# Kernel optimization log

Hardware: AMD Instinct MI355X
Metric: run time of the kernel (lower is better)

Reference implementation:

```python
import jax, jax.numpy as jnp
import numpy as np

B, S, F = 32, 8, 4
N0, N1, N2 = 2048, 4096, 2048
H, OUT = 1024, 256
IN = N0 + N1 + N2  # 8192
SC_LAYERS = 2


def setup_inputs() -> dict:
    key = jax.random.key(0)
    ks = jax.random.split(key, 16)
    rn = jax.random.normal
    inp = {
        'xs0': rn(ks[0], (B, S, N0), jnp.float32),
        'xs1': rn(ks[1], (B, S, N1), jnp.float32),
        'xs2': rn(ks[2], (B, S, N2), jnp.float32),
        # dense Laplacians, scaled so L@x keeps unit-ish variance
        'L0': rn(ks[3], (N0, N0), jnp.float32) / np.sqrt(N0).astype(np.float32),
        'L1': rn(ks[4], (N1, N1), jnp.float32) / np.sqrt(N1).astype(np.float32),
        'L2': rn(ks[5], (N2, N2), jnp.float32) / np.sqrt(N2).astype(np.float32),
        # per-layer, per-filter diagonal weights (std=0.01 as in torch init)
        'Wc0': 0.01 * rn(ks[6], (SC_LAYERS, F, N0), jnp.float32),
        'Wc1': 0.01 * rn(ks[7], (SC_LAYERS, F, N1), jnp.float32),
        'Wc2': 0.01 * rn(ks[8], (SC_LAYERS, F, N2), jnp.float32),
        # MLP params (xavier-ish)
        'W_in': rn(ks[9], (IN, H), jnp.float32) / np.sqrt(IN).astype(np.float32),
        'b_in': jnp.zeros((H,), jnp.float32),
        'W_h': rn(ks[10], (H, H), jnp.float32) / np.sqrt(H).astype(np.float32),
        'b_h': jnp.zeros((H,), jnp.float32),
        'W_out': rn(ks[11], (H, OUT), jnp.float32) / np.sqrt(H).astype(np.float32),
        'b_out': jnp.zeros((OUT,), jnp.float32),
    }
    return inp


def _conv_stack(x, L, Wc):
    # x: [B, S, n]; L: [n, n]; Wc: [layers, F, n]
    for l in range(Wc.shape[0]):
        # batched Laplacian matmul: (L @ x_bs) for every (b, s)
        Lx = jnp.einsum('bsn,mn->bsm', x, L)  # [B, S, n]
        # diagonal filter scaling + activation + sum over filters (fused)
        x = jax.nn.relu(Lx[:, :, None, :] * Wc[l][None, None, :, :]).sum(axis=2)
    return x


def reference(xs0, xs1, xs2, L0, L1, L2, Wc0, Wc1, Wc2,
              W_in, b_in, W_h, b_h, W_out, b_out):
    h = jnp.concatenate([
        _conv_stack(xs0, L0, Wc0),
        _conv_stack(xs1, L1, Wc1),
        _conv_stack(xs2, L2, Wc2),
    ], axis=-1)                      # [B, S, IN]
    h = h.sum(axis=1)                # sum over sequence -> [B, IN]
    h = jax.nn.relu(h @ W_in + b_in)
    h = jax.nn.relu(h @ W_h + b_h)   # single hidden layer (nn_layers=2)
    return h @ W_out + b_out         # [B, OUT]
```

## Files before the change

### kernel.cpp

```cpp
#include <hip/hip_runtime.h>
#include <hip/hip_bf16.h>


#define B_    32
#define S_    8
#define BS_   256
#define F_    4
#define IN_   8192
#define H_    1024
#define OUT_  256

#define L_TOT  25165824LL
#define LOFF1  4194304LL
#define LOFF2  20971520LL

#define PF_B1  2097152LL
#define PF_B2  10485760LL
#define PF_TOT 12582912LL

typedef __attribute__((ext_vector_type(8)))  short bf16x8;
typedef __attribute__((ext_vector_type(4)))  short short4v;
typedef __attribute__((ext_vector_type(8)))  short short8v;
typedef __attribute__((ext_vector_type(16))) float f32x16;
typedef __attribute__((ext_vector_type(4)))  float f32x4;

typedef const __attribute__((address_space(1))) void* gas_ptr;
typedef __attribute__((address_space(3))) void* las_ptr;

__device__ __forceinline__ void gload16(const void* g, void* s) {
    __builtin_amdgcn_global_load_lds((gas_ptr)g, (las_ptr)s, 16, 0, 0);
}

__device__ __forceinline__ unsigned short rne_bf16(float f) {
    unsigned int u = __builtin_bit_cast(unsigned int, f);
    u += 0x7FFFu + ((u >> 16) & 1u);
    return (unsigned short)(u >> 16);
}

__global__ void k_pre(const float* __restrict__ L0, const float* __restrict__ L1,
                      const float* __restrict__ L2, unsigned short* __restrict__ Lb,
                      const float* __restrict__ x0, const float* __restrict__ x1,
                      const float* __restrict__ x2,
                      unsigned short* __restrict__ Xhi, unsigned short* __restrict__ Xlo,
                      const float* __restrict__ Wc0, const float* __restrict__ Wc1,
                      const float* __restrict__ Wc2, float* __restrict__ PM)
{
    const int bx = blockIdx.x, tid = threadIdx.x;
    if (bx < 3072) {
        const long long b0 = (long long)bx * 8192;
        const float* src; long long off;
        if (b0 < LOFF1)      { src = L0; off = 0; }
        else if (b0 < LOFF2) { src = L1; off = LOFF1; }
        else                 { src = L2; off = LOFF2; }
        const float* pb = src + (b0 - off) + tid * 8;
        #pragma unroll
        for (int u = 0; u < 4; ++u) {
            const float* p = pb + u * 2048;
            f32x4 a = __builtin_nontemporal_load((const f32x4*)p);
            f32x4 b = __builtin_nontemporal_load((const f32x4*)p + 1);
            short8v o;
            o[0] = (short)rne_bf16(a.x); o[1] = (short)rne_bf16(a.y);
            o[2] = (short)rne_bf16(a.z); o[3] = (short)rne_bf16(a.w);
            o[4] = (short)rne_bf16(b.x); o[5] = (short)rne_bf16(b.y);
            o[6] = (short)rne_bf16(b.z); o[7] = (short)rne_bf16(b.w);
            *(short8v*)(Lb + b0 + u * 2048 + tid * 8) = o;
        }
    } else if (bx < 3584) {
        const int base = (bx - 3072) * 4096 + tid * 8;
        #pragma unroll
        for (int u = 0; u < 2; ++u) {
            int e = base + u * 2048;
            int m = e >> 13, c = e & 8191;
            const float* src; int n, c0;
            if (c < 2048)      { src = x0; n = 2048; c0 = c; }
            else if (c < 6144) { src = x1; n = 4096; c0 = c - 2048; }
            else               { src = x2; n = 2048; c0 = c - 6144; }
            const float* p = src + (size_t)m * n + c0;
            f32x4 a = __builtin_nontemporal_load((const f32x4*)p);
            f32x4 b = __builtin_nontemporal_load((const f32x4*)p + 1);
            float v[8] = {a.x, a.y, a.z, a.w, b.x, b.y, b.z, b.w};
            short8v h, l;
            #pragma unroll
            for (int i = 0; i < 8; ++i) {
                unsigned short hb = rne_bf16(v[i]);
                float hf = __builtin_bit_cast(float, (unsigned int)hb << 16);
                h[i] = (short)hb;
                l[i] = (short)rne_bf16(v[i] - hf);
            }
            *(short8v*)(Xhi + (size_t)m * IN_ + c) = h;
            *(short8v*)(Xlo + (size_t)m * IN_ + c) = l;
        }
    } else {
        const int base = (bx - 3584) * 2048 + tid * 8;
        #pragma unroll
        for (int i = 0; i < 8; ++i) {
            int idx = base + i;
            int l = idx / IN_, n = idx % IN_;
            const float* Wc; int nb, j;
            if (n < 2048)      { Wc = Wc0; nb = 2048; j = n;        }
            else if (n < 6144) { Wc = Wc1; nb = 4096; j = n - 2048; }
            else               { Wc = Wc2; nb = 2048; j = n - 6144; }
            float p = 0.f, m = 0.f;
            #pragma unroll
            for (int f = 0; f < F_; ++f) {
                float w = Wc[(l * F_ + f) * nb + j];
                p += fmaxf(w, 0.f);
                m += fmaxf(-w, 0.f);
            }
            PM[(l * 2 + 0) * IN_ + n] = p;
            PM[(l * 2 + 1) * IN_ + n] = m;
        }
    }
}

__global__ __launch_bounds__(256, 2) void k_gemm(
    const unsigned short* __restrict__ Xhi, const unsigned short* __restrict__ Xlo,
    const unsigned short* __restrict__ Lb,
    float* __restrict__ pf)
{
    __shared__ __attribute__((aligned(16))) unsigned short Ah[2][128 * 32];
    __shared__ __attribute__((aligned(16))) unsigned short Al[2][128 * 32];
    __shared__ __attribute__((aligned(16))) unsigned short Bs[2][256 * 32];

    const int bx = blockIdx.x;
    int n_, noff, mt, nt, sk, ld; long long loff; size_t pbase;
    if (bx < 256) {
        int u = bx;
        int j = (u & 7) | ((u >> 4) << 3);
        nt = j >> 3; sk = j & 7; mt = (u >> 3) & 1;
        n_ = 4096; noff = 2048; loff = LOFF1; pbase = PF_B1; ld = 4096;
    } else if (bx < 320) {
        int u = bx - 256;
        int j = (u & 7) | ((u >> 4) << 3);
        nt = j >> 2; sk = j & 3; mt = (u >> 3) & 1;
        n_ = 2048; noff = 0; loff = 0; pbase = 0; ld = 2048;
    } else {
        int u = bx - 320;
        int j = (u & 7) | ((u >> 4) << 3);
        nt = j >> 2; sk = j & 3; mt = (u >> 3) & 1;
        n_ = 2048; noff = 6144; loff = LOFF2; pbase = PF_B2; ld = 2048;
    }
    const int k0 = sk * 512;

    const int tid = threadIdx.x;

    const int sg = ((tid & 3) ^ ((tid >> 3) & 3)) << 3;
    const unsigned short* gAh = Xhi + (size_t)(mt * 128 + (tid >> 2)) * IN_ + noff + k0 + sg;
    const unsigned short* gAl = Xlo + (size_t)(mt * 128 + (tid >> 2)) * IN_ + noff + k0 + sg;
    const unsigned short* gB  = Lb + loff + (size_t)(nt * 256 + (tid >> 2)) * n_ + k0 + sg;
    const size_t a64 = (size_t)64 * IN_, b64 = (size_t)64 * n_;
    const int tb = tid * 16;

    #define STAGE(buf, ko)                                                      \
        do {                                                                    \
            char* pa = (char*)&Ah[buf][0];                                      \
            char* pl = (char*)&Al[buf][0];                                      \
            char* pb = (char*)&Bs[buf][0];                                      \
            gload16(gAh + (ko),       pa + tb);                                 \
            gload16(gAh + (ko) + a64, pa + 4096 + tb);                          \
            gload16(gAl + (ko),       pl + tb);                                 \
            gload16(gAl + (ko) + a64, pl + 4096 + tb);                          \
            gload16(gB + (ko),           pb + tb);                              \
            gload16(gB + (ko) + b64,     pb + 4096 + tb);                       \
            gload16(gB + (ko) + 2 * b64, pb + 8192 + tb);                       \
            gload16(gB + (ko) + 3 * b64, pb + 12288 + tb);                      \
        } while (0)

    const int l = tid & 63, w = tid >> 6;
    const int l31 = l & 31, lh = l >> 5;
    const int wm = w >> 1, wn = w & 1;
    const int swz = (l31 >> 1) & 3;

    f32x16 acc[2][4];
    #pragma unroll
    for (int r = 0; r < 2; ++r)
        #pragma unroll
        for (int c = 0; c < 4; ++c)
            #pragma unroll
            for (int e = 0; e < 16; ++e) acc[r][c][e] = 0.f;

    STAGE(0, 0);
    STAGE(1, 32);

    for (int it = 0; it < 16; ++it) {
        if (it < 15) asm volatile("s_waitcnt vmcnt(8)" ::: "memory");
        else         asm volatile("s_waitcnt vmcnt(0)" ::: "memory");
        __builtin_amdgcn_s_barrier();
        asm volatile("" ::: "memory");

        const int cur = it & 1;
        const unsigned short* cA = &Ah[cur][0];
        const unsigned short* cL = &Al[cur][0];
        const unsigned short* cB = &Bs[cur][0];
        __builtin_amdgcn_s_setprio(1);
        #pragma unroll
        for (int t = 0; t < 2; ++t) {
            const int sidx = (((t << 1) + lh) ^ swz) << 3;
            bf16x8 fah[2], fal[2], fb[4];
            #pragma unroll
            for (int r = 0; r < 2; ++r) {
                fah[r] = *(const bf16x8*)&cA[(wm * 64 + r * 32 + l31) * 32 + sidx];
                fal[r] = *(const bf16x8*)&cL[(wm * 64 + r * 32 + l31) * 32 + sidx];
            }
            #pragma unroll
            for (int c = 0; c < 4; ++c)
                fb[c] = *(const bf16x8*)&cB[(wn * 128 + c * 32 + l31) * 32 + sidx];
            #pragma unroll
            for (int r = 0; r < 2; ++r)
                #pragma unroll
                for (int c = 0; c < 4; ++c) {
                    acc[r][c] = __builtin_amdgcn_mfma_f32_32x32x16_bf16(fal[r], fb[c], acc[r][c], 0, 0, 0);
                    acc[r][c] = __builtin_amdgcn_mfma_f32_32x32x16_bf16(fah[r], fb[c], acc[r][c], 0, 0, 0);
                }
        }
        __builtin_amdgcn_s_setprio(0);
        asm volatile("" ::: "memory");
        __builtin_amdgcn_s_barrier();

        if (it + 2 < 16) STAGE(cur, (it + 2) * 32);
        asm volatile("" ::: "memory");
    }
    #undef STAGE

    const int colL = nt * 256 + wn * 128 + l31;
    float* pw = pf + pbase + (size_t)sk * 256 * ld;
    #pragma unroll
    for (int r = 0; r < 2; ++r) {
        const int rowb = mt * 128 + wm * 64 + r * 32 + 4 * lh;
        #pragma unroll
        for (int e = 0; e < 16; ++e) {
            const int row = rowb + (e & 3) + 8 * (e >> 2);
            #pragma unroll
            for (int c = 0; c < 4; ++c)
                pw[(size_t)row * ld + colL + c * 32] = acc[r][c][e];
        }
    }
}

__device__ __forceinline__ void pf_decode(int c, size_t& base, int& nsl, int& ld, int& cl) {
    if (c < 2048)      { base = 0;      nsl = 4; ld = 2048; cl = c; }
    else if (c < 6144) { base = PF_B1;  nsl = 8; ld = 4096; cl = c - 2048; }
    else               { base = PF_B2;  nsl = 4; ld = 2048; cl = c - 6144; }
}

__global__ void k_epi0(const float* __restrict__ pf,
                       const float* __restrict__ Pv, const float* __restrict__ Mv,
                       unsigned short* __restrict__ Yhi, unsigned short* __restrict__ Ylo) {
    int e = (blockIdx.x * 256 + threadIdx.x) * 4;
    int m = e >> 13, c = e & 8191;
    size_t base; int nsl, ld, cl;
    pf_decode(c, base, nsl, ld, cl);
    const float* p0 = pf + base + (size_t)m * ld + cl;
    const size_t sstr = (size_t)256 * ld;
    float vs[4] = {0.f, 0.f, 0.f, 0.f};
    for (int s = 0; s < nsl; ++s) {
        float4 v = *(const float4*)(p0 + (size_t)s * sstr);
        vs[0] += v.x; vs[1] += v.y; vs[2] += v.z; vs[3] += v.w;
    }
    float4 pv = *(const float4*)(Pv + c);
    float4 mv = *(const float4*)(Mv + c);
    float pa[4] = {pv.x, pv.y, pv.z, pv.w};
    float ma[4] = {mv.x, mv.y, mv.z, mv.w};
    short hv[4], lv[4];
    #pragma unroll
    for (int j = 0; j < 4; ++j) {
        float y = fmaxf(vs[j], 0.f) * pa[j] + fmaxf(-vs[j], 0.f) * ma[j];
        unsigned short hb = rne_bf16(y);
        float hf = __builtin_bit_cast(float, (unsigned int)hb << 16);
        hv[j] = (short)hb;
        lv[j] = (short)rne_bf16(y - hf);
    }
    short4v h = {hv[0], hv[1], hv[2], hv[3]};
    short4v lo = {lv[0], lv[1], lv[2], lv[3]};
    *(short4v*)(Yhi + (size_t)m * IN_ + c) = h;
    *(short4v*)(Ylo + (size_t)m * IN_ + c) = lo;
}

__global__ void k_epi1s(const float* __restrict__ pf,
                        const float* __restrict__ Pv, const float* __restrict__ Mv,
                        float* __restrict__ hsum) {
    int e = (blockIdx.x * 256 + threadIdx.x) * 4;
    int b = e >> 13, c = e & 8191;
    size_t base; int nsl, ld, cl;
    pf_decode(c, base, nsl, ld, cl);
    const size_t sstr = (size_t)256 * ld;
    float4 pv = *(const float4*)(Pv + c);
    float4 mv = *(const float4*)(Mv + c);
    float pa[4] = {pv.x, pv.y, pv.z, pv.w};
    float ma[4] = {mv.x, mv.y, mv.z, mv.w};
    float hs[4] = {0.f, 0.f, 0.f, 0.f};
    for (int q = 0; q < 8; ++q) {
        const int m = b * 8 + q;
        const float* p0 = pf + base + (size_t)m * ld + cl;
        float vs[4] = {0.f, 0.f, 0.f, 0.f};
        for (int s = 0; s < nsl; ++s) {
            float4 v = *(const float4*)(p0 + (size_t)s * sstr);
            vs[0] += v.x; vs[1] += v.y; vs[2] += v.z; vs[3] += v.w;
        }
        #pragma unroll
        for (int j = 0; j < 4; ++j)
            hs[j] += fmaxf(vs[j], 0.f) * pa[j] + fmaxf(-vs[j], 0.f) * ma[j];
    }
    *(float4*)(hsum + (size_t)b * IN_ + c) = *(float4*)hs;
}

template<int KC>
__global__ __launch_bounds__(256) void k_mlp3(
    const float* __restrict__ X, const float* __restrict__ W,
    float* __restrict__ P, int K, int H)
{
    __shared__ float Xs[32][KC];
    const int tid = threadIdx.x;
    const int lane = tid & 63;
    const int mg = tid >> 6;
    const int h = (blockIdx.x * 64 + lane) * 4;
    const int c = blockIdx.y, k0 = c * KC;

    for (int i = tid * 4; i < 32 * KC; i += 1024) {
        int m = i / KC, kk = i % KC;
        *(float4*)&Xs[m][kk] = *(const float4*)(X + (size_t)m * K + k0 + kk);
    }
    __syncthreads();

    float4 acc[8];
    #pragma unroll
    for (int m = 0; m < 8; ++m) acc[m] = {0.f, 0.f, 0.f, 0.f};

    const float* wp = W + (size_t)k0 * H + h;
    for (int kk = 0; kk < KC; kk += 4) {
        float4 w4[4];
        #pragma unroll
        for (int u = 0; u < 4; ++u)
            w4[u] = *(const float4*)(wp + (size_t)(kk + u) * H);
        #pragma unroll
        for (int m = 0; m < 8; ++m) {
            float4 xv = *(const float4*)&Xs[mg * 8 + m][kk];
            acc[m].x = fmaf(xv.x, w4[0].x, acc[m].x);
            acc[m].y = fmaf(xv.x, w4[0].y, acc[m].y);
            acc[m].z = fmaf(xv.x, w4[0].z, acc[m].z);
            acc[m].w = fmaf(xv.x, w4[0].w, acc[m].w);
            acc[m].x = fmaf(xv.y, w4[1].x, acc[m].x);
            acc[m].y = fmaf(xv.y, w4[1].y, acc[m].y);
            acc[m].z = fmaf(xv.y, w4[1].z, acc[m].z);
            acc[m].w = fmaf(xv.y, w4[1].w, acc[m].w);
            acc[m].x = fmaf(xv.z, w4[2].x, acc[m].x);
            acc[m].y = fmaf(xv.z, w4[2].y, acc[m].y);
            acc[m].z = fmaf(xv.z, w4[2].z, acc[m].z);
            acc[m].w = fmaf(xv.z, w4[2].w, acc[m].w);
            acc[m].x = fmaf(xv.w, w4[3].x, acc[m].x);
            acc[m].y = fmaf(xv.w, w4[3].y, acc[m].y);
            acc[m].z = fmaf(xv.w, w4[3].z, acc[m].z);
            acc[m].w = fmaf(xv.w, w4[3].w, acc[m].w);
        }
    }
    #pragma unroll
    for (int m = 0; m < 8; ++m)
        *(float4*)(P + ((size_t)c * 32 + mg * 8 + m) * H + h) = acc[m];
}

__global__ void k_reduce4(const float* __restrict__ P, const float* __restrict__ bias,
                          float* __restrict__ Y, int NC, int MH4, int H, int do_relu) {
    int idx = blockIdx.x * 256 + threadIdx.x;
    if (idx >= MH4) return;
    int h0 = (idx * 4) % H;
    float4 s = *(const float4*)(bias + h0);
    for (int c = 0; c < NC; ++c) {
        float4 v = *(const float4*)(P + (size_t)c * MH4 * 4 + (size_t)idx * 4);
        s.x += v.x; s.y += v.y; s.z += v.z; s.w += v.w;
    }
    if (do_relu) {
        s.x = fmaxf(s.x, 0.f); s.y = fmaxf(s.y, 0.f);
        s.z = fmaxf(s.z, 0.f); s.w = fmaxf(s.w, 0.f);
    }
    *(float4*)(Y + (size_t)idx * 4) = s;
}

extern "C" void kernel_launch(void* const* d_in, const int* in_sizes, int n_in,
                              void* d_out, int out_size, void* d_ws, size_t ws_size,
                              hipStream_t stream) {
    const float* xs0  = (const float*)d_in[0];
    const float* xs1  = (const float*)d_in[1];
    const float* xs2  = (const float*)d_in[2];
    const float* L0   = (const float*)d_in[3];
    const float* L1   = (const float*)d_in[4];
    const float* L2   = (const float*)d_in[5];
    const float* Wc0  = (const float*)d_in[6];
    const float* Wc1  = (const float*)d_in[7];
    const float* Wc2  = (const float*)d_in[8];
    const float* W_in = (const float*)d_in[9];
    const float* b_in = (const float*)d_in[10];
    const float* W_h  = (const float*)d_in[11];
    const float* b_h  = (const float*)d_in[12];
    const float* W_out= (const float*)d_in[13];
    const float* b_out= (const float*)d_in[14];

    char* w = (char*)d_ws;
    float*          PM  = (float*)w;          w += (size_t)4 * IN_ * 4;
    unsigned short* Lb  = (unsigned short*)w; w += (size_t)L_TOT * 2;
    unsigned short* Xhi = (unsigned short*)w; w += (size_t)BS_ * IN_ * 2;
    unsigned short* Xlo = (unsigned short*)w; w += (size_t)BS_ * IN_ * 2;
    float*          pf  = (float*)w;          w += (size_t)PF_TOT * 4;
    float*          hsum= (float*)w;          w += (size_t)32 * IN_ * 4;
    float*          p1  = pf;
    float*          h1  = (float*)w;          w += (size_t)32 * H_ * 4;
    float*          p2  = (float*)w;          w += (size_t)32 * 32 * H_ * 4;
    float*          h2  = (float*)w;          w += (size_t)32 * H_ * 4;
    float*          p3  = (float*)w;          w += (size_t)32 * 32 * OUT_ * 4;
    unsigned short* Yhi = Xhi;
    unsigned short* Ylo = Xlo;

    k_pre<<<3592, 256, 0, stream>>>(L0, L1, L2, Lb, xs0, xs1, xs2, Xhi, Xlo,
                                    Wc0, Wc1, Wc2, PM);

    k_gemm<<<384, 256, 0, stream>>>(Xhi, Xlo, Lb, pf);
    k_epi0<<<2048, 256, 0, stream>>>(pf, PM + 0 * IN_, PM + 1 * IN_, Yhi, Ylo);
    k_gemm<<<384, 256, 0, stream>>>(Yhi, Ylo, Lb, pf);
    k_epi1s<<<256, 256, 0, stream>>>(pf, PM + 2 * IN_, PM + 3 * IN_, hsum);

    {
        dim3 g(4, 128);
        k_mlp3<64><<<g, 256, 0, stream>>>(hsum, W_in, p1, IN_, H_);
        k_reduce4<<<32, 256, 0, stream>>>(p1, b_in, h1, 128, 8192, H_, 1);
    }
    {
        dim3 g(4, 32);
        k_mlp3<32><<<g, 256, 0, stream>>>(h1, W_h, p2, H_, H_);
        k_reduce4<<<32, 256, 0, stream>>>(p2, b_h, h2, 32, 8192, H_, 1);
    }
    {
        dim3 g(1, 32);
        k_mlp3<32><<<g, 256, 0, stream>>>(h2, W_out, p3, H_, OUT_);
        k_reduce4<<<8, 256, 0, stream>>>(p3, b_out, (float*)d_out, 32, 2048, OUT_, 0);
    }
}
```

Baseline: 223.2 us.

## Rework Laplacian GEMM into 512-thread blocks with 4-stage LDS pipeline and halved split-K

The Laplacian GEMM now runs 192 blocks of 512 threads (8 waves, each computing a 64x64 sub-tile) instead of 384 blocks of 256 threads. Split-K is halved, so each block covers 1024 of K and the partial-sum buffer and epilogue reductions shrink by half. Loads now go through a 4-stage LDS ring with A and B issues interleaved between half-step MFMA groups and register double-buffered fragments. The aim is to reduce partial-sum traffic and hide load latency better. The cost is fewer blocks, which may leave some of the 256 CUs idle, and more LDS per block.

```diff
diff --git a/kernel.cpp b/kernel.cpp
--- a/kernel.cpp
+++ b/kernel.cpp
@@ -14,9 +14,9 @@
 #define LOFF1  4194304LL
 #define LOFF2  20971520LL
 
-#define PF_B1  2097152LL
-#define PF_B2  10485760LL
-#define PF_TOT 12582912LL
+#define PF_B1  1048576LL
+#define PF_B2  5242880LL
+#define PF_TOT 6291456LL
 
 typedef __attribute__((ext_vector_type(8)))  short bf16x8;
 typedef __attribute__((ext_vector_type(4)))  short short4v;
@@ -113,134 +113,133 @@
     }
 }
 
-__global__ __launch_bounds__(256, 2) void k_gemm(
+struct Frag6 { bf16x8 ah0, ah1, al0, al1, b0, b1; };
+
+__global__ __launch_bounds__(512, 1) void k_gemm(
     const unsigned short* __restrict__ Xhi, const unsigned short* __restrict__ Xlo,
     const unsigned short* __restrict__ Lb,
     float* __restrict__ pf)
 {
-    __shared__ __attribute__((aligned(16))) unsigned short Ah[2][128 * 32];
-    __shared__ __attribute__((aligned(16))) unsigned short Al[2][128 * 32];
-    __shared__ __attribute__((aligned(16))) unsigned short Bs[2][256 * 32];
+    __shared__ __attribute__((aligned(16))) char lds[4 * 32768];
 
     const int bx = blockIdx.x;
     int n_, noff, mt, nt, sk, ld; long long loff; size_t pbase;
-    if (bx < 256) {
-        int u = bx;
-        int j = (u & 7) | ((u >> 4) << 3);
-        nt = j >> 3; sk = j & 7; mt = (u >> 3) & 1;
+    if (bx < 128) {
+        sk = bx & 3; int v = bx >> 2; mt = v & 1; nt = v >> 1;
         n_ = 4096; noff = 2048; loff = LOFF1; pbase = PF_B1; ld = 4096;
-    } else if (bx < 320) {
-        int u = bx - 256;
-        int j = (u & 7) | ((u >> 4) << 3);
-        nt = j >> 2; sk = j & 3; mt = (u >> 3) & 1;
+    } else if (bx < 160) {
+        int u = bx - 128; sk = u & 1; mt = (u >> 1) & 1; nt = u >> 2;
         n_ = 2048; noff = 0; loff = 0; pbase = 0; ld = 2048;
     } else {
-        int u = bx - 320;
-        int j = (u & 7) | ((u >> 4) << 3);
-        nt = j >> 2; sk = j & 3; mt = (u >> 3) & 1;
+        int u = bx - 160; sk = u & 1; mt = (u >> 1) & 1; nt = u >> 2;
         n_ = 2048; noff = 6144; loff = LOFF2; pbase = PF_B2; ld = 2048;
     }
-    const int k0 = sk * 512;
+    const int k0 = sk << 10;
 
     const int tid = threadIdx.x;
 
     const int sg = ((tid & 3) ^ ((tid >> 3) & 3)) << 3;
-    const unsigned short* gAh = Xhi + (size_t)(mt * 128 + (tid >> 2)) * IN_ + noff + k0 + sg;
-    const unsigned short* gAl = Xlo + (size_t)(mt * 128 + (tid >> 2)) * IN_ + noff + k0 + sg;
-    const unsigned short* gB  = Lb + loff + (size_t)(nt * 256 + (tid >> 2)) * n_ + k0 + sg;
-    const size_t a64 = (size_t)64 * IN_, b64 = (size_t)64 * n_;
+    const unsigned short* gA = Xhi + (size_t)(mt * 128 + (tid >> 2)) * IN_ + noff + k0 + sg;
+    const unsigned short* gL = Xlo + (size_t)(mt * 128 + (tid >> 2)) * IN_ + noff + k0 + sg;
+    const unsigned short* gB = Lb + loff + (size_t)(nt * 256 + (tid >> 2)) * n_ + k0 + sg;
+    const unsigned short* gB2 = gB + (size_t)128 * n_;
     const int tb = tid * 16;
-
-    #define STAGE(buf, ko)                                                      \
-        do {                                                                    \
-            char* pa = (char*)&Ah[buf][0];                                      \
-            char* pl = (char*)&Al[buf][0];                                      \
-            char* pb = (char*)&Bs[buf][0];                                      \
-            gload16(gAh + (ko),       pa + tb);                                 \
-            gload16(gAh + (ko) + a64, pa + 4096 + tb);                          \
-            gload16(gAl + (ko),       pl + tb);                                 \
-            gload16(gAl + (ko) + a64, pl + 4096 + tb);                          \
-            gload16(gB + (ko),           pb + tb);                              \
-            gload16(gB + (ko) + b64,     pb + 4096 + tb);                       \
-            gload16(gB + (ko) + 2 * b64, pb + 8192 + tb);                       \
-            gload16(gB + (ko) + 3 * b64, pb + 12288 + tb);                      \
-        } while (0)
+    char* lb = lds;
+
+    #define ISS_A(u) do { const int _s = (u) & 3; const int _ko = (u) * 32;     \
+        gload16(gA + _ko, lb + _s * 32768 + tb);                                \
+        gload16(gL + _ko, lb + _s * 32768 + 8192 + tb); } while (0)
+    #define ISS_B(u) do { const int _s = (u) & 3; const int _ko = (u) * 32;     \
+        gload16(gB + _ko,  lb + _s * 32768 + 16384 + tb);                       \
+        gload16(gB2 + _ko, lb + _s * 32768 + 24576 + tb); } while (0)
 
     const int l = tid & 63, w = tid >> 6;
     const int l31 = l & 31, lh = l >> 5;
-    const int wm = w >> 1, wn = w & 1;
+    const int wm = w >> 2, wn = w & 3;
     const int swz = (l31 >> 1) & 3;
-
-    f32x16 acc[2][4];
+    const int rA0 = (wm * 64 + l31) * 64;
+    const int rB0 = (wn * 64 + l31) * 64;
+
+    f32x16 a00, a01, a10, a11;
     #pragma unroll
-    for (int r = 0; r < 2; ++r)
-        #pragma unroll
-        for (int c = 0; c < 4; ++c)
-            #pragma unroll
-            for (int e = 0; e < 16; ++e) acc[r][c][e] = 0.f;
-
-    STAGE(0, 0);
-    STAGE(1, 32);
-
-    for (int it = 0; it < 16; ++it) {
-        if (it < 15) asm volatile("s_waitcnt vmcnt(8)" ::: "memory");
-        else         asm volatile("s_waitcnt vmcnt(0)" ::: "memory");
+    for (int r = 0; r < 16; ++r) { a00[r] = 0.f; a01[r] = 0.f; a10[r] = 0.f; a11[r] = 0.f; }
+
+    #define READ6(Fv, s, j) do {                                                \
+        const int _se = ((((j) * 2 + lh) ^ swz) << 4);                          \
+        const char* _b = lb + (s) * 32768;                                      \
+        Fv.ah0 = *(const bf16x8*)(_b + rA0 + _se);                              \
+        Fv.ah1 = *(const bf16x8*)(_b + rA0 + 2048 + _se);                       \
+        Fv.al0 = *(const bf16x8*)(_b + 8192 + rA0 + _se);                       \
+        Fv.al1 = *(const bf16x8*)(_b + 8192 + rA0 + 2048 + _se);                \
+        Fv.b0  = *(const bf16x8*)(_b + 16384 + rB0 + _se);                      \
+        Fv.b1  = *(const bf16x8*)(_b + 16384 + rB0 + 2048 + _se); } while (0)
+
+    #define MFMA8(Fv) do {                                                      \
+        __builtin_amdgcn_s_setprio(1);                                          \
+        a00 = __builtin_amdgcn_mfma_f32_32x32x16_bf16(Fv.al0, Fv.b0, a00, 0, 0, 0); \
+        a00 = __builtin_amdgcn_mfma_f32_32x32x16_bf16(Fv.ah0, Fv.b0, a00, 0, 0, 0); \
+        a01 = __builtin_amdgcn_mfma_f32_32x32x16_bf16(Fv.al0, Fv.b1, a01, 0, 0, 0); \
+        a01 = __builtin_amdgcn_mfma_f32_32x32x16_bf16(Fv.ah0, Fv.b1, a01, 0, 0, 0); \
+        a10 = __builtin_amdgcn_mfma_f32_32x32x16_bf16(Fv.al1, Fv.b0, a10, 0, 0, 0); \
+        a10 = __builtin_amdgcn_mfma_f32_32x32x16_bf16(Fv.ah1, Fv.b0, a10, 0, 0, 0); \
+        a11 = __builtin_amdgcn_mfma_f32_32x32x16_bf16(Fv.al1, Fv.b1, a11, 0, 0, 0); \
+        a11 = __builtin_amdgcn_mfma_f32_32x32x16_bf16(Fv.ah1, Fv.b1, a11, 0, 0, 0); \
+        __builtin_amdgcn_s_setprio(0); } while (0)
+
+    ISS_A(0); ISS_B(0);
+    ISS_A(1); ISS_B(1);
+    ISS_A(2); ISS_B(2);
+    asm volatile("s_waitcnt vmcnt(8)" ::: "memory");
+    __builtin_amdgcn_s_barrier();
+    asm volatile("" ::: "memory");
+
+    Frag6 F0, F1;
+    READ6(F0, 0, 0);
+
+    for (int u = 0; u < 32; ++u) {
+        const int s = u & 3;
+        READ6(F1, s, 1);
+        if (u + 3 < 32) ISS_A(u + 3);
+        MFMA8(F0);
+        if (u <= 28)      asm volatile("s_waitcnt vmcnt(6)" ::: "memory");
+        else if (u == 29) asm volatile("s_waitcnt vmcnt(4)" ::: "memory");
+        else if (u == 30) asm volatile("s_waitcnt vmcnt(0)" ::: "memory");
         __builtin_amdgcn_s_barrier();
         asm volatile("" ::: "memory");
 
-        const int cur = it & 1;
-        const unsigned short* cA = &Ah[cur][0];
-        const unsigned short* cL = &Al[cur][0];
-        const unsigned short* cB = &Bs[cur][0];
-        __builtin_amdgcn_s_setprio(1);
-        #pragma unroll
-        for (int t = 0; t < 2; ++t) {
-            const int sidx = (((t << 1) + lh) ^ swz) << 3;
-            bf16x8 fah[2], fal[2], fb[4];
-            #pragma unroll
-            for (int r = 0; r < 2; ++r) {
-                fah[r] = *(const bf16x8*)&cA[(wm * 64 + r * 32 + l31) * 32 + sidx];
-                fal[r] = *(const bf16x8*)&cL[(wm * 64 + r * 32 + l31) * 32 + sidx];
-            }
-            #pragma unroll
-            for (int c = 0; c < 4; ++c)
-                fb[c] = *(const bf16x8*)&cB[(wn * 128 + c * 32 + l31) * 32 + sidx];
-            #pragma unroll
-            for (int r = 0; r < 2; ++r)
-                #pragma unroll
-                for (int c = 0; c < 4; ++c) {
-                    acc[r][c] = __builtin_amdgcn_mfma_f32_32x32x16_bf16(fal[r], fb[c], acc[r][c], 0, 0, 0);
-                    acc[r][c] = __builtin_amdgcn_mfma_f32_32x32x16_bf16(fah[r], fb[c], acc[r][c], 0, 0, 0);
-                }
-        }
-        __builtin_amdgcn_s_setprio(0);
-        asm volatile("" ::: "memory");
-        __builtin_amdgcn_s_barrier();
-
-        if (it + 2 < 16) STAGE(cur, (it + 2) * 32);
-        asm volatile("" ::: "memory");
-    }
-    #undef STAGE
-
-    const int colL = nt * 256 + wn * 128 + l31;
+        if (u + 1 < 32) READ6(F0, (u + 1) & 3, 0);
+        if (u + 3 < 32) ISS_B(u + 3);
+        MFMA8(F1);
+        if (u + 1 < 32) {
+            __builtin_amdgcn_s_barrier();
+            asm volatile("" ::: "memory");
+        }
+    }
+    #undef READ6
+    #undef MFMA8
+    #undef ISS_A
+    #undef ISS_B
+
+    const int colb = nt * 256 + wn * 64 + l31;
     float* pw = pf + pbase + (size_t)sk * 256 * ld;
     #pragma unroll
-    for (int r = 0; r < 2; ++r) {
-        const int rowb = mt * 128 + wm * 64 + r * 32 + 4 * lh;
+    for (int rb = 0; rb < 2; ++rb) {
+        const int rowb = mt * 128 + wm * 64 + rb * 32 + 4 * lh;
+        const f32x16& c0 = rb ? a10 : a00;
+        const f32x16& c1 = rb ? a11 : a01;
         #pragma unroll
         for (int e = 0; e < 16; ++e) {
             const int row = rowb + (e & 3) + 8 * (e >> 2);
-            #pragma unroll
-            for (int c = 0; c < 4; ++c)
-                pw[(size_t)row * ld + colL + c * 32] = acc[r][c][e];
+            pw[(size_t)row * ld + colb]      = c0[e];
+            pw[(size_t)row * ld + colb + 32] = c1[e];
         }
     }
 }
 
 __device__ __forceinline__ void pf_decode(int c, size_t& base, int& nsl, int& ld, int& cl) {
-    if (c < 2048)      { base = 0;      nsl = 4; ld = 2048; cl = c; }
-    else if (c < 6144) { base = PF_B1;  nsl = 8; ld = 4096; cl = c - 2048; }
-    else               { base = PF_B2;  nsl = 4; ld = 2048; cl = c - 6144; }
+    if (c < 2048)      { base = 0;      nsl = 2; ld = 2048; cl = c; }
+    else if (c < 6144) { base = PF_B1;  nsl = 4; ld = 4096; cl = c - 2048; }
+    else               { base = PF_B2;  nsl = 2; ld = 2048; cl = c - 6144; }
 }
 
 __global__ void k_epi0(const float* __restrict__ pf,
@@ -412,9 +411,9 @@
     k_pre<<<3592, 256, 0, stream>>>(L0, L1, L2, Lb, xs0, xs1, xs2, Xhi, Xlo,
                                     Wc0, Wc1, Wc2, PM);
 
-    k_gemm<<<384, 256, 0, stream>>>(Xhi, Xlo, Lb, pf);
+    k_gemm<<<192, 512, 0, stream>>>(Xhi, Xlo, Lb, pf);
     k_epi0<<<2048, 256, 0, stream>>>(pf, PM + 0 * IN_, PM + 1 * IN_, Yhi, Ylo);
-    k_gemm<<<384, 256, 0, stream>>>(Yhi, Ylo, Lb, pf);
+    k_gemm<<<192, 512, 0, stream>>>(Yhi, Ylo, Lb, pf);
     k_epi1s<<<256, 256, 0, stream>>>(pf, PM + 2 * IN_, PM + 3 * IN_, hsum);
 
     {
```

Measured after the change: 203.6 us. -8.8%, faster.

## Widen GEMM tile to 512 columns with 8 waves and triple-buffered LDS pipeline

Applied to the files above, without the earlier changes.

The Laplacian GEMM kernel moves to 512-thread blocks, each computing a 128x512 output tile, which halves the grid to 192 blocks. Shared memory becomes a three-stage ring of 48KB buffers, and each K-step's global loads are split into two halves interleaved with the two MFMA phases. The aim is to overlap memory traffic with compute and to reuse the A operand across more output columns. The cost is one block per CU with fewer blocks than CUs, so occupancy drops and latency hiding depends on the pipeline.

```diff
diff --git a/kernel.cpp b/kernel.cpp
--- a/kernel.cpp
+++ b/kernel.cpp
@@ -113,31 +113,23 @@
     }
 }
 
-__global__ __launch_bounds__(256, 2) void k_gemm(
+__global__ __launch_bounds__(512, 1) void k_gemm(
     const unsigned short* __restrict__ Xhi, const unsigned short* __restrict__ Xlo,
     const unsigned short* __restrict__ Lb,
     float* __restrict__ pf)
 {
-    __shared__ __attribute__((aligned(16))) unsigned short Ah[2][128 * 32];
-    __shared__ __attribute__((aligned(16))) unsigned short Al[2][128 * 32];
-    __shared__ __attribute__((aligned(16))) unsigned short Bs[2][256 * 32];
+    __shared__ __attribute__((aligned(16))) char lds[3 * 49152];
 
     const int bx = blockIdx.x;
     int n_, noff, mt, nt, sk, ld; long long loff; size_t pbase;
-    if (bx < 256) {
-        int u = bx;
-        int j = (u & 7) | ((u >> 4) << 3);
-        nt = j >> 3; sk = j & 7; mt = (u >> 3) & 1;
+    if (bx < 128) {
+        sk = bx & 7; int v = bx >> 3; mt = v & 1; nt = v >> 1;
         n_ = 4096; noff = 2048; loff = LOFF1; pbase = PF_B1; ld = 4096;
-    } else if (bx < 320) {
-        int u = bx - 256;
-        int j = (u & 7) | ((u >> 4) << 3);
-        nt = j >> 2; sk = j & 3; mt = (u >> 3) & 1;
+    } else if (bx < 160) {
+        int u = bx - 128; sk = u & 3; mt = (u >> 2) & 1; nt = u >> 3;
         n_ = 2048; noff = 0; loff = 0; pbase = 0; ld = 2048;
     } else {
-        int u = bx - 320;
-        int j = (u & 7) | ((u >> 4) << 3);
-        nt = j >> 2; sk = j & 3; mt = (u >> 3) & 1;
+        int u = bx - 160; sk = u & 3; mt = (u >> 2) & 1; nt = u >> 3;
         n_ = 2048; noff = 6144; loff = LOFF2; pbase = PF_B2; ld = 2048;
     }
     const int k0 = sk * 512;
@@ -147,92 +139,99 @@
     const int sg = ((tid & 3) ^ ((tid >> 3) & 3)) << 3;
     const unsigned short* gAh = Xhi + (size_t)(mt * 128 + (tid >> 2)) * IN_ + noff + k0 + sg;
     const unsigned short* gAl = Xlo + (size_t)(mt * 128 + (tid >> 2)) * IN_ + noff + k0 + sg;
-    const unsigned short* gB  = Lb + loff + (size_t)(nt * 256 + (tid >> 2)) * n_ + k0 + sg;
-    const size_t a64 = (size_t)64 * IN_, b64 = (size_t)64 * n_;
+    const unsigned short* gB  = Lb + loff + (size_t)(nt * 512 + (tid >> 2)) * n_ + k0 + sg;
+    const size_t b128r = (size_t)128 * n_;
     const int tb = tid * 16;
 
-    #define STAGE(buf, ko)                                                      \
-        do {                                                                    \
-            char* pa = (char*)&Ah[buf][0];                                      \
-            char* pl = (char*)&Al[buf][0];                                      \
-            char* pb = (char*)&Bs[buf][0];                                      \
-            gload16(gAh + (ko),       pa + tb);                                 \
-            gload16(gAh + (ko) + a64, pa + 4096 + tb);                          \
-            gload16(gAl + (ko),       pl + tb);                                 \
-            gload16(gAl + (ko) + a64, pl + 4096 + tb);                          \
-            gload16(gB + (ko),           pb + tb);                              \
-            gload16(gB + (ko) + b64,     pb + 4096 + tb);                       \
-            gload16(gB + (ko) + 2 * b64, pb + 8192 + tb);                       \
-            gload16(gB + (ko) + 3 * b64, pb + 12288 + tb);                      \
-        } while (0)
+    #define ISS_H1(s, ko) do { char* _b = lds + (s) * 49152;                     \
+        gload16(gAh + (ko), _b + tb);                                            \
+        gload16(gAl + (ko), _b + 8192 + tb);                                     \
+        gload16(gB + (ko),  _b + 16384 + tb); } while (0)
+    #define ISS_H2(s, ko) do { char* _b = lds + (s) * 49152;                     \
+        gload16(gB + (ko) + b128r,     _b + 16384 + 8192 + tb);                  \
+        gload16(gB + (ko) + 2 * b128r, _b + 16384 + 16384 + tb);                 \
+        gload16(gB + (ko) + 3 * b128r, _b + 16384 + 24576 + tb); } while (0)
 
     const int l = tid & 63, w = tid >> 6;
     const int l31 = l & 31, lh = l >> 5;
-    const int wm = w >> 1, wn = w & 1;
+    const int wm = w >> 2, wn = w & 3;
     const int swz = (l31 >> 1) & 3;
+    int aoff[2], boff[4];
+    #pragma unroll
+    for (int rb = 0; rb < 2; ++rb) aoff[rb] = (wm * 64 + rb * 32 + l31) * 64;
+    #pragma unroll
+    for (int cb = 0; cb < 4; ++cb) boff[cb] = 16384 + (wn * 128 + cb * 32 + l31) * 64;
 
     f32x16 acc[2][4];
     #pragma unroll
-    for (int r = 0; r < 2; ++r)
-        #pragma unroll
-        for (int c = 0; c < 4; ++c)
+    for (int rb = 0; rb < 2; ++rb)
+        #pragma unroll
+        for (int cb = 0; cb < 4; ++cb)
             #pragma unroll
-            for (int e = 0; e < 16; ++e) acc[r][c][e] = 0.f;
-
-    STAGE(0, 0);
-    STAGE(1, 32);
+            for (int e = 0; e < 16; ++e) acc[rb][cb][e] = 0.f;
+
+    #define PHASE(s, j) do {                                                     \
+        const char* _b = lds + (s) * 49152;                                      \
+        const int _sl = ((((j) * 2 + lh) ^ swz) << 4);                           \
+        bf16x8 fah[2], fal[2], fb[4];                                            \
+        _Pragma("unroll")                                                        \
+        for (int rb = 0; rb < 2; ++rb) {                                         \
+            fah[rb] = *(const bf16x8*)(_b + aoff[rb] + _sl);                     \
+            fal[rb] = *(const bf16x8*)(_b + 8192 + aoff[rb] + _sl);              \
+        }                                                                        \
+        _Pragma("unroll")                                                        \
+        for (int cb = 0; cb < 4; ++cb)                                           \
+            fb[cb] = *(const bf16x8*)(_b + boff[cb] + _sl);                      \
+        __builtin_amdgcn_s_setprio(1);                                           \
+        _Pragma("unroll")                                                        \
+        for (int rb = 0; rb < 2; ++rb)                                           \
+            _Pragma("unroll")                                                    \
+            for (int cb = 0; cb < 4; ++cb) {                                     \
+                acc[rb][cb] = __builtin_amdgcn_mfma_f32_32x32x16_bf16(fal[rb], fb[cb], acc[rb][cb], 0, 0, 0); \
+                acc[rb][cb] = __builtin_amdgcn_mfma_f32_32x32x16_bf16(fah[rb], fb[cb], acc[rb][cb], 0, 0, 0); \
+            }                                                                    \
+        __builtin_amdgcn_s_setprio(0); } while (0)
+
+    ISS_H1(0, 0); ISS_H2(0, 0);
+    ISS_H1(1, 32); ISS_H2(1, 32);
+    asm volatile("s_waitcnt vmcnt(6)" ::: "memory");
+    __builtin_amdgcn_s_barrier();
+    asm volatile("" ::: "memory");
 
     for (int it = 0; it < 16; ++it) {
-        if (it < 15) asm volatile("s_waitcnt vmcnt(8)" ::: "memory");
-        else         asm volatile("s_waitcnt vmcnt(0)" ::: "memory");
+        const int cur = it % 3;
+        const int nxt = (it + 2) % 3;
+        const int ko = (it + 2) * 32;
+
+        if (it + 2 < 16) ISS_H1(nxt, ko);
+        __builtin_amdgcn_sched_barrier(0);
+        PHASE(cur, 0);
         __builtin_amdgcn_s_barrier();
         asm volatile("" ::: "memory");
 
-        const int cur = it & 1;
-        const unsigned short* cA = &Ah[cur][0];
-        const unsigned short* cL = &Al[cur][0];
-        const unsigned short* cB = &Bs[cur][0];
-        __builtin_amdgcn_s_setprio(1);
-        #pragma unroll
-        for (int t = 0; t < 2; ++t) {
-            const int sidx = (((t << 1) + lh) ^ swz) << 3;
-            bf16x8 fah[2], fal[2], fb[4];
-            #pragma unroll
-            for (int r = 0; r < 2; ++r) {
-                fah[r] = *(const bf16x8*)&cA[(wm * 64 + r * 32 + l31) * 32 + sidx];
-                fal[r] = *(const bf16x8*)&cL[(wm * 64 + r * 32 + l31) * 32 + sidx];
-            }
-            #pragma unroll
-            for (int c = 0; c < 4; ++c)
-                fb[c] = *(const bf16x8*)&cB[(wn * 128 + c * 32 + l31) * 32 + sidx];
-            #pragma unroll
-            for (int r = 0; r < 2; ++r)
-                #pragma unroll
-                for (int c = 0; c < 4; ++c) {
-                    acc[r][c] = __builtin_amdgcn_mfma_f32_32x32x16_bf16(fal[r], fb[c], acc[r][c], 0, 0, 0);
-                    acc[r][c] = __builtin_amdgcn_mfma_f32_32x32x16_bf16(fah[r], fb[c], acc[r][c], 0, 0, 0);
-                }
-        }
-        __builtin_amdgcn_s_setprio(0);
+        if (it + 2 < 16) ISS_H2(nxt, ko);
+        __builtin_amdgcn_sched_barrier(0);
+        PHASE(cur, 1);
+
+        if (it < 14)       asm volatile("s_waitcnt vmcnt(6)" ::: "memory");
+        else if (it == 14) asm volatile("s_waitcnt vmcnt(0)" ::: "memory");
+        __builtin_amdgcn_s_barrier();
         asm volatile("" ::: "memory");
-        __builtin_amdgcn_s_barrier();
-
-        if (it + 2 < 16) STAGE(cur, (it + 2) * 32);
-        asm volatile("" ::: "memory");
-    }
-    #undef STAGE
-
-    const int colL = nt * 256 + wn * 128 + l31;
+    }
+    #undef PHASE
+    #undef ISS_H1
+    #undef ISS_H2
+
     float* pw = pf + pbase + (size_t)sk * 256 * ld;
     #pragma unroll
-    for (int r = 0; r < 2; ++r) {
-        const int rowb = mt * 128 + wm * 64 + r * 32 + 4 * lh;
+    for (int rb = 0; rb < 2; ++rb) {
+        const int rowb = mt * 128 + wm * 64 + rb * 32 + 4 * lh;
         #pragma unroll
         for (int e = 0; e < 16; ++e) {
             const int row = rowb + (e & 3) + 8 * (e >> 2);
             #pragma unroll
-            for (int c = 0; c < 4; ++c)
-                pw[(size_t)row * ld + colL + c * 32] = acc[r][c][e];
+            for (int cb = 0; cb < 4; ++cb)
+                pw[(size_t)row * ld + nt * 512 + wn * 128 + cb * 32 + l31] = acc[rb][cb][e];
         }
     }
 }
@@ -412,9 +411,9 @@
     k_pre<<<3592, 256, 0, stream>>>(L0, L1, L2, Lb, xs0, xs1, xs2, Xhi, Xlo,
                                     Wc0, Wc1, Wc2, PM);
 
-    k_gemm<<<384, 256, 0, stream>>>(Xhi, Xlo, Lb, pf);
+    k_gemm<<<192, 512, 0, stream>>>(Xhi, Xlo, Lb, pf);
     k_epi0<<<2048, 256, 0, stream>>>(pf, PM + 0 * IN_, PM + 1 * IN_, Yhi, Ylo);
-    k_gemm<<<384, 256, 0, stream>>>(Yhi, Ylo, Lb, pf);
+    k_gemm<<<192, 512, 0, stream>>>(Yhi, Ylo, Lb, pf);
     k_epi1s<<<256, 256, 0, stream>>>(pf, PM + 2 * IN_, PM + 3 * IN_, hsum);
 
     {
```

New measurement: 221.8 us. Within noise of the previous version (-0.6%).
